# Kernel tuning notes

Hardware: AMD Instinct MI355X
Metric: run time of the kernel (lower is better)

The kernel has to match this reference:

```python
import jax, jax.numpy as jnp
import numpy as np

A, Bc, C, D = 32, 16, 16, 16
K, PAD = 3, 1
KK = K * K
KKA = KK * A            # 288
KKA2 = KKA // 2 + 1     # 145
BSZ, H, W = 4, 14, 14


def unfold(x, k, pad):
    # torch F.unfold ordering: channel-major, kernel-minor -> matches patches
    p = jax.lax.conv_general_dilated_patches(
        x, (k, k), (1, 1), padding=((pad, pad), (pad, pad)),
        dimension_numbers=("NCHW", "OIHW", "NCHW"))
    b, ckk, h, w = p.shape
    return p.reshape(b, ckk, h * w)


def freq_filter(x, cw):
    # x: [bl, kkA, B, D]; shared complex filter over all B splits (Frequency)
    xf = jnp.fft.rfft(x.astype(jnp.float32), axis=1, norm='ortho')  # [bl,kkA2,B,D]
    wc = cw[..., 0] + 1j * cw[..., 1]                               # [kkA2, D]
    y = jnp.fft.irfft(xf * wc[None, :, None, :], n=x.shape[1], axis=1, norm='ortho')
    return y + x


def spatial_gate(logit, gamma, beta, w, bias):
    # logit: [bl, kkA, B]; shared Spatial module applied per B split (vectorized)
    bl, kka, nb = logit.shape
    g = logit.reshape(bl, KK, A, nb)
    mu = g.mean(axis=2, keepdims=True)
    var = g.var(axis=2, keepdims=True)
    g = (g - mu) / jnp.sqrt(var + 1e-5) * gamma[None, None, :, None] + beta[None, None, :, None]
    # conv1d with kernel size 1 == channel mixing over kk
    out = jnp.einsum('oi,biaj->boaj', w, g) + bias[None, :, None, None]
    out = jax.nn.gelu(out, approximate=False)
    return out.reshape(bl, kka, nb) + logit  # residual inside Spatial


def setup_inputs():
    key = jax.random.key(0)
    ks = jax.random.split(key, 8)
    return {
        "a": jax.random.uniform(ks[0], (BSZ, A, H, W), jnp.float32) + 0.1,
        "pose": jax.random.normal(ks[1], (BSZ, A * C, H, W), jnp.float32),
        "mpose_w": jax.random.normal(ks[2], (Bc * D, C), jnp.float32) * 0.05,
        "mpose_b": jnp.zeros((Bc * D,), jnp.float32),
        "cpose2_w": jax.random.normal(ks[3], (Bc, C), jnp.float32) * 0.05,
        "cpose2_b": jnp.zeros((Bc,), jnp.float32),
        "complex_weight": jax.random.normal(ks[4], (KKA2, C, 2), jnp.float32) * 0.02,
        "ln_gamma": jnp.ones((A,), jnp.float32),
        "ln_beta": jnp.zeros((A,), jnp.float32),
        "sp_w": jax.random.normal(ks[5], (KK, KK), jnp.float32) * 0.1,
        "sp_b": jnp.ones((KK,), jnp.float32),
    }


def reference(a, pose, mpose_w, mpose_b, cpose2_w, cpose2_b, complex_weight,
              ln_gamma, ln_beta, sp_w, sp_b):
    b, _, h, w = a.shape
    # ---- unfold pose: [b, A*C*kk, l] -> [b*l, kkA, C]
    pu = unfold(pose, K, PAD)
    l = pu.shape[-1]
    pu = pu.reshape(b, A, C, KK, l).transpose(0, 4, 3, 1, 2).reshape(b * l, KKA, C)
    # ---- pose transform + frequency filter
    p = jax.nn.gelu(pu @ mpose_w.T + mpose_b, approximate=False)
    p = freq_filter(p.reshape(b * l, KKA, Bc, D), complex_weight)
    pose_out = p.reshape(b, l, KKA, Bc, D)
    # ---- routing logits: linear + (spatial gate + residual) added to logit
    logit = pu @ cpose2_w.T + cpose2_b                      # [bl, kkA, B]
    logit = logit + spatial_gate(logit, ln_gamma, ln_beta, sp_w, sp_b)
    r = jax.nn.softmax(logit, axis=2).reshape(b, l, KKA, Bc)
    # ---- unfold activations: [b, l, kkA, 1]
    au = unfold(a, K, PAD).reshape(b, A, KK, l).transpose(0, 3, 2, 1).reshape(b, l, KKA, 1)
    ar = au * r                                             # [b,l,kkA,B]
    ar_sum = ar.sum(axis=2, keepdims=True)                  # [b,l,1,B]
    coeff = (ar / ar_sum)[..., None]                        # [b,l,kkA,B,1]
    a_out = (ar_sum / au.sum(axis=2, keepdims=True)).squeeze(2)  # [b,l,B]
    a_out = a_out.transpose(0, 2, 1).reshape(b, Bc, h, w)
    po = (coeff * pose_out).sum(axis=2).reshape(b, l, Bc * D)
    po = po.transpose(0, 2, 1).reshape(b, Bc * D, h, w)
    return a_out, po
```

## Files before the change

kernel.cpp:

```cpp
#include <hip/hip_runtime.h>
#include <math.h>


typedef __attribute__((ext_vector_type(8))) short bf16x8;
typedef __attribute__((ext_vector_type(4))) float f32x4;

__device__ inline float4 ld4(const float* p) { return *reinterpret_cast<const float4*>(p); }
__device__ inline void st4(float* p, float4 v) { *reinterpret_cast<float4*>(p) = v; }
__device__ inline unsigned short f2bf(float f) {
  union { float f; unsigned int i; } v; v.f = f;
  unsigned int r = v.i + 0x7FFFu + ((v.i >> 16) & 1u);
  return (unsigned short)(r >> 16);
}
__device__ inline float gelu_f(float v) {
  float u = v * 0.70710678118654752f;
  float au = fabsf(u);
  float t = __builtin_amdgcn_rcpf(fmaf(0.3275911f, au, 1.f));
  float poly = t * fmaf(t, fmaf(t, fmaf(t, fmaf(t, 1.061405429f, -1.453152027f),
                                        1.421413741f), -0.284496736f),
                        0.254829592f);
  float e = __expf(-u * u);
  float r = fmaf(-poly, e, 1.f);
  float erfv = copysignf(r, u);
  return 0.5f * v * (1.f + erfv);
}

__global__ __launch_bounds__(256) void k_prep(
    const float* __restrict__ cw, const float* __restrict__ pose,
    const float* __restrict__ a_img, unsigned short* __restrict__ ws_H,
    float* __restrict__ poseT, float* __restrict__ aT) {
  int bid = blockIdx.x, tid = threadIdx.x;
  if (bid < 96) {
    __shared__ float s_h2[576];
    __shared__ float s_cs[288], s_sn[288], s_wr[145], s_wi[145];
    int d = bid / 6, chunk = bid % 6;
    for (int m = tid; m < 288; m += 256) {
      float sn, cs;
      sincosf((float)m * (6.283185307179586f / 288.f), &sn, &cs);
      s_cs[m] = cs; s_sn[m] = sn;
    }
    for (int f = tid; f < 145; f += 256) {
      s_wr[f] = cw[(f * 16 + d) * 2 + 0];
      s_wi[f] = cw[(f * 16 + d) * 2 + 1];
    }
    __syncthreads();
    for (int t = tid; t < 288; t += 256) {
      float acc = s_wr[0] + ((t & 1) ? -s_wr[144] : s_wr[144]);
      for (int f = 1; f < 144; ++f) {
        int m = (f * t) % 288;
        acc = fmaf(2.f * s_wr[f], s_cs[m], acc);
        acc = fmaf(-2.f * s_wi[f], s_sn[m], acc);
      }
      float h = acc * (1.f / 288.f);
      s_h2[t] = h;
      s_h2[t + 288] = h;
    }
    __syncthreads();
    for (int e = tid; e < 13824; e += 256) {
      int j = e & 7, l = (e >> 3) & 63;
      int kk = (e >> 9) % 9, mtl = (e >> 9) / 9;
      int mt = chunk * 3 + mtl;
      int m = l & 15, g = l >> 4;
      int n = kk * 32 + g * 8 + j, t = mt * 16 + m;
      float v = s_h2[n - t + 288] + ((n == t) ? 1.f : 0.f);
      ws_H[d * 82944 + ((mt * 9 + kk) * 64 + l) * 8 + j] = f2bf(v);
    }
  } else {
    __shared__ float s[32 * 201];
    int tb = bid - 96;
    int b = tb / 17, ch = tb % 17;
    const float* src = (ch < 16) ? (pose + (b * 512 + ch * 32) * 196)
                                 : (a_img + b * 32 * 196);
    for (int e = tid; e < 6272; e += 256) {
      int c = e / 196, l = e - c * 196;
      s[c * 201 + l] = src[e];
    }
    __syncthreads();
    if (ch < 16) {
      float* dst = poseT + b * 196 * 512 + ch * 32;
      for (int e = tid; e < 6272; e += 256) {
        int l = e >> 5, c = e & 31;
        dst[l * 512 + c] = s[c * 201 + l];
      }
    } else {
      float* dst = aT + b * 196 * 32;
      for (int e = tid; e < 6272; e += 256) {
        int l = e >> 5, c = e & 31;
        dst[l * 32 + c] = s[c * 201 + l];
      }
    }
  }
}

__global__ __launch_bounds__(256) void k_rowprep(
    const float* __restrict__ poseT, const float* __restrict__ aT,
    const float* __restrict__ cpose2_w, const float* __restrict__ cpose2_b,
    const float* __restrict__ ln_g, const float* __restrict__ ln_b,
    const float* __restrict__ sp_w, const float* __restrict__ sp_b,
    float* __restrict__ out_a, unsigned short* __restrict__ ws_pu,
    unsigned short* __restrict__ ws_cb) {
  __shared__ __align__(16) float s_pu[288 * 20];
#define s_l2 s_pu
  __shared__ __align__(16) float s_lg[288 * 20];
  __shared__ float s_au[288];
  __shared__ float s_mu[144], s_rs[144];
  __shared__ float s_ga[32], s_be[32];
  __shared__ float s_part[256], s_pau[16];
  __shared__ float s_as[16];

  int tid = threadIdx.x;
  int row = blockIdx.x;
  int b = row / 196, loc = row % 196, i0 = loc / 14, j0 = loc % 14;
  int b_ = tid & 15;

  if (tid < 32) { s_ga[tid] = ln_g[tid]; s_be[tid] = ln_b[tid]; }

  float wcol[16];
#pragma unroll
  for (int q = 0; q < 4; ++q) {
    float4 v = ld4(&cpose2_w[b_ * 16 + 4 * q]);
    wcol[4 * q] = v.x; wcol[4 * q + 1] = v.y;
    wcol[4 * q + 2] = v.z; wcol[4 * q + 3] = v.w;
  }
  float cbv = cpose2_b[b_];

  const float* pT = poseT + b * 196 * 512;
  for (int e = tid; e < 1152; e += 256) {
    int q = e & 3, n = e >> 2;
    int kk = n >> 5, a = n & 31;
    int ki = (kk * 11) >> 5, kj = kk - 3 * ki;
    int yy = i0 + ki - 1, xx = j0 + kj - 1;
    float4 v = make_float4(0.f, 0.f, 0.f, 0.f);
    if ((unsigned)yy < 14u && (unsigned)xx < 14u)
      v = ld4(&pT[(yy * 14 + xx) * 512 + a * 16 + q * 4]);
    st4(&s_pu[n * 20 + q * 4], v);
  }
  const float* aTb = aT + b * 196 * 32;
  for (int n = tid; n < 288; n += 256) {
    int kk = n >> 5, a = n & 31;
    int ki = (kk * 11) >> 5, kj = kk - 3 * ki;
    int yy = i0 + ki - 1, xx = j0 + kj - 1;
    float v = 0.f;
    if ((unsigned)yy < 14u && (unsigned)xx < 14u)
      v = aTb[(yy * 14 + xx) * 32 + a];
    s_au[n] = v;
  }
  __syncthreads();

  for (int e = tid; e < 4608; e += 256) {
    int j = e & 7, l2 = (e >> 3) & 31, mt = e >> 8;
    int m = l2 & 15, c = (l2 >> 4) * 8 + j;
    ws_pu[row * 4608 + e] = f2bf(s_pu[(mt * 16 + m) * 20 + c]);
  }

  {
    int n0 = tid >> 4;
#pragma unroll 3
    for (int k = 0; k < 18; ++k) {
      int n = n0 + 16 * k;
      const float* pr = &s_pu[n * 20];
      float acc = cbv;
#pragma unroll
      for (int q = 0; q < 4; ++q) {
        float4 p = ld4(pr + 4 * q);
        acc += p.x * wcol[4 * q] + p.y * wcol[4 * q + 1] +
               p.z * wcol[4 * q + 2] + p.w * wcol[4 * q + 3];
      }
      s_lg[n * 20 + b_] = acc;
    }
  }
  __syncthreads();

  if (tid < 144) {
    int kk = tid >> 4, B = tid & 15;
    float s = 0.f, s2 = 0.f;
    for (int a = 0; a < 32; ++a) {
      float v = s_lg[(kk * 32 + a) * 20 + B];
      s += v; s2 += v * v;
    }
    float mu = s * (1.f / 32.f);
    float var = s2 * (1.f / 32.f) - mu * mu;
    s_mu[tid] = mu;
    s_rs[tid] = rsqrtf(var + 1e-5f);
  } else if (tid < 160) {
    int t2 = tid - 144;
    float p = 0.f;
    for (int i = 0; i < 18; ++i) p += s_au[t2 * 18 + i];
    s_pau[t2] = p;
  }
  __syncthreads();

  {
    float mu9[9], rs9[9];
#pragma unroll
    for (int i2 = 0; i2 < 9; ++i2) {
      mu9[i2] = s_mu[i2 * 16 + b_];
      rs9[i2] = s_rs[i2 * 16 + b_];
    }
#pragma unroll
    for (int half = 0; half < 2; ++half) {
      int a = (tid >> 4) + 16 * half;
      float ga = s_ga[a], be = s_be[a];
      float gn[9], lg9[9];
#pragma unroll
      for (int i2 = 0; i2 < 9; ++i2) {
        float v = s_lg[(i2 * 32 + a) * 20 + b_];
        lg9[i2] = v;
        gn[i2] = (v - mu9[i2]) * rs9[i2] * ga + be;
      }
#pragma unroll
      for (int o = 0; o < 9; ++o) {
        float acc = sp_b[o];
#pragma unroll
        for (int i2 = 0; i2 < 9; ++i2) acc += sp_w[o * 9 + i2] * gn[i2];
        s_l2[(o * 32 + a) * 20 + b_] = 2.f * lg9[o] + gelu_f(acc);
      }
    }
  }
  __syncthreads();

  for (int n = tid; n < 288; n += 256) {
    float v[16];
#pragma unroll
    for (int q = 0; q < 4; ++q) {
      float4 t = ld4(&s_l2[n * 20 + 4 * q]);
      v[4 * q] = t.x; v[4 * q + 1] = t.y; v[4 * q + 2] = t.z; v[4 * q + 3] = t.w;
    }
    float m = v[0];
#pragma unroll
    for (int e = 1; e < 16; ++e) m = fmaxf(m, v[e]);
    float s = 0.f;
#pragma unroll
    for (int e = 0; e < 16; ++e) { v[e] = __expf(v[e] - m); s += v[e]; }
    float inv = 1.f / s;
#pragma unroll
    for (int q = 0; q < 4; ++q)
      st4(&s_l2[n * 20 + 4 * q],
          make_float4(v[4 * q] * inv, v[4 * q + 1] * inv, v[4 * q + 2] * inv,
                      v[4 * q + 3] * inv));
  }
  __syncthreads();

  {
    int sl = tid >> 4;
    float part = 0.f;
#pragma unroll 3
    for (int i = 0; i < 18; ++i) {
      int n = sl * 18 + i;
      part += s_au[n] * s_l2[n * 20 + b_];
    }
    s_part[tid] = part;
  }
  __syncthreads();

  if (tid < 16) {
    float s = 0.f;
#pragma unroll
    for (int q = 0; q < 16; ++q) s += s_part[tid + 16 * q];
    s_as[tid] = s;
    float aus = 0.f;
#pragma unroll
    for (int q = 0; q < 16; ++q) aus += s_pau[q];
    out_a[(b * 16 + tid) * 196 + loc] = s / aus;
  }
  __syncthreads();

  {
    float inv_as = 1.f / s_as[(tid >> 3) & 15];
    for (int e = tid; e < 4608; e += 256) {
      int j = e & 7, B = (e >> 3) & 15, g2 = (e >> 7) & 3, kk = e >> 9;
      int n = kk * 32 + g2 * 8 + j;
      float v = s_au[n] * s_l2[n * 20 + B] * inv_as;
      ws_cb[row * 4608 + e] = f2bf(v);
    }
  }
#undef s_l2
}

__global__ __launch_bounds__(256, 3) void k_gterm(
    const unsigned short* __restrict__ ws_H,
    const unsigned short* __restrict__ ws_pu,
    const unsigned short* __restrict__ ws_cb,
    const float* __restrict__ mpose_w, const float* __restrict__ mpose_b,
    float* __restrict__ out_po) {
  int bid = blockIdx.x;
  int xcd = bid & 7, q = bid >> 3;
  int k13 = q % 13, d = q / 13;
  int ro = xcd + 8 * k13;
  if (ro >= 98) return;

  int tid = threadIdx.x;
  int w = tid >> 6, l = tid & 63;
  int row0 = ro * 8 + w * 2, row1 = row0 + 1;
  int b_ = l & 15, g = l >> 4;

  const bf16x8 z8 = {0, 0, 0, 0, 0, 0, 0, 0};
  const f32x4 zf = {0.f, 0.f, 0.f, 0.f};

  bf16x8 bmw = z8;
  if (g < 2) {
    const float* mp = mpose_w + (b_ * 16 + d) * 16 + g * 8;
#pragma unroll
    for (int j = 0; j < 8; ++j) bmw[j] = (short)f2bf(mp[j]);
  }
  float mb = mpose_b[b_ * 16 + d];

  union CU { uint4 u; bf16x8 v; };
  CU c0[9], c1[9];
  {
    const uint4* gC0 = (const uint4*)ws_cb + row0 * 576;
    const uint4* gC1 = (const uint4*)ws_cb + row1 * 576;
#pragma unroll
    for (int kk = 0; kk < 9; ++kk) {
      c0[kk].u = gC0[kk * 64 + l];
      c1[kk].u = gC1[kk * 64 + l];
    }
#pragma unroll
    for (int kk = 0; kk < 9; ++kk) {
      asm volatile("" : "+v"(c0[kk].u.x), "+v"(c0[kk].u.y),
                        "+v"(c0[kk].u.z), "+v"(c0[kk].u.w));
      asm volatile("" : "+v"(c1[kk].u.x), "+v"(c1[kk].u.y),
                        "+v"(c1[kk].u.z), "+v"(c1[kk].u.w));
    }
  }
  const bf16x8* aP0 = (const bf16x8*)ws_pu + row0 * 576;
  const bf16x8* aP1 = (const bf16x8*)ws_pu + row1 * 576;
  const bf16x8* aH = (const bf16x8*)ws_H + d * 10368;

  bf16x8 an0 = z8, an1 = z8;
  if (g < 2) { an0 = aP0[l]; an1 = aP1[l]; }

  float po0 = 0.f, po1 = 0.f;
  for (int mt = 0; mt < 18; ++mt) {
    bf16x8 h[9];
#pragma unroll
    for (int kk = 0; kk < 9; ++kk) h[kk] = aH[(mt * 9 + kk) * 64 + l];
    bf16x8 a0 = an0, a1 = an1;
    if (mt < 17 && g < 2) {
      an0 = aP0[(mt + 1) * 32 + l];
      an1 = aP1[(mt + 1) * 32 + l];
    }
    __builtin_amdgcn_s_setprio(1);
    f32x4 xp0 = __builtin_amdgcn_mfma_f32_16x16x32_bf16(a0, bmw, zf, 0, 0, 0);
    f32x4 xp1 = __builtin_amdgcn_mfma_f32_16x16x32_bf16(a1, bmw, zf, 0, 0, 0);
    f32x4 g0a = zf, g0b = zf, g1a = zf, g1b = zf;
#pragma unroll
    for (int kp = 0; kp < 4; ++kp) {
      g0a = __builtin_amdgcn_mfma_f32_16x16x32_bf16(h[2 * kp], c0[2 * kp].v, g0a, 0, 0, 0);
      g1a = __builtin_amdgcn_mfma_f32_16x16x32_bf16(h[2 * kp], c1[2 * kp].v, g1a, 0, 0, 0);
      g0b = __builtin_amdgcn_mfma_f32_16x16x32_bf16(h[2 * kp + 1], c0[2 * kp + 1].v, g0b, 0, 0, 0);
      g1b = __builtin_amdgcn_mfma_f32_16x16x32_bf16(h[2 * kp + 1], c1[2 * kp + 1].v, g1b, 0, 0, 0);
    }
    g0a = __builtin_amdgcn_mfma_f32_16x16x32_bf16(h[8], c0[8].v, g0a, 0, 0, 0);
    g1a = __builtin_amdgcn_mfma_f32_16x16x32_bf16(h[8], c1[8].v, g1a, 0, 0, 0);
    __builtin_amdgcn_s_setprio(0);
#pragma unroll
    for (int r = 0; r < 4; ++r) {
      float s0 = xp0[r] + mb, s1 = xp1[r] + mb;
      float x0 = gelu_f(s0), x1 = gelu_f(s1);
      po0 = fmaf(g0a[r], x0, po0);
      po0 = fmaf(g0b[r], x0, po0);
      po1 = fmaf(g1a[r], x1, po1);
      po1 = fmaf(g1b[r], x1, po1);
    }
  }

  po0 += __shfl_xor(po0, 16);
  po0 += __shfl_xor(po0, 32);
  po1 += __shfl_xor(po1, 16);
  po1 += __shfl_xor(po1, 32);
  if (l < 16) {
    int bb = row0 / 196, lc0 = row0 % 196, lc1 = row1 % 196;
    out_po[((bb * 256) + l * 16 + d) * 196 + lc0] = po0;
    out_po[((bb * 256) + l * 16 + d) * 196 + lc1] = po1;
  }
}

extern "C" void kernel_launch(void* const* d_in, const int* in_sizes, int n_in,
                              void* d_out, int out_size, void* d_ws, size_t ws_size,
                              hipStream_t stream) {
  const float* a_img    = (const float*)d_in[0];
  const float* pose     = (const float*)d_in[1];
  const float* mpose_w  = (const float*)d_in[2];
  const float* mpose_b  = (const float*)d_in[3];
  const float* cpose2_w = (const float*)d_in[4];
  const float* cpose2_b = (const float*)d_in[5];
  const float* cw       = (const float*)d_in[6];
  const float* ln_g     = (const float*)d_in[7];
  const float* ln_b     = (const float*)d_in[8];
  const float* sp_w     = (const float*)d_in[9];
  const float* sp_b     = (const float*)d_in[10];

  float* out = (float*)d_out;
  float* poseT  = (float*)d_ws;
  float* aT     = poseT + 4 * 196 * 512;
  unsigned short* ws_H  = (unsigned short*)(aT + 4 * 196 * 32);
  unsigned short* ws_pu = ws_H + 16 * 82944;
  unsigned short* ws_cb = ws_pu + 784 * 4608;

  hipLaunchKernelGGL(k_prep, dim3(164), dim3(256), 0, stream,
                     cw, pose, a_img, ws_H, poseT, aT);
  hipLaunchKernelGGL(k_rowprep, dim3(784), dim3(256), 0, stream,
                     poseT, aT, cpose2_w, cpose2_b, ln_g, ln_b, sp_w, sp_b,
                     out, ws_pu, ws_cb);
  hipLaunchKernelGGL(k_gterm, dim3(1664), dim3(256), 0, stream,
                     ws_H, ws_pu, ws_cb, mpose_w, mpose_b, out + 12544);
}
```

Measured before the change: 117.8 us.

## Remap rowprep rows to match gterm XCD layout and simplify MFMA chains

k_rowprep now uses the same XCD-aware block-to-row mapping as k_gterm, so each row's ws_pu/ws_cb data is written on the XCD whose L2 will later read it. Its grid grows to 832 blocks, with the excess blocks exiting early. In k_gterm the bias is folded into the MFMA accumulator input. The two interleaved accumulator chains are merged into one serial chain of 9 MFMAs per row, and setprio is removed. The single chain lengthens MFMA dependency latency while cutting register use and a few adds.

```diff
diff --git a/kernel.cpp b/kernel.cpp
--- a/kernel.cpp
+++ b/kernel.cpp
@@ -108,8 +108,13 @@
   __shared__ float s_part[256], s_pau[16];
   __shared__ float s_as[16];
 
+  int bid = blockIdx.x;
+  int x = bid & 7, j = bid >> 3;
+  int o = x + 8 * (j % 13);
+  if (o >= 98) return;
+  int row = o * 8 + (j / 13);
+
   int tid = threadIdx.x;
-  int row = blockIdx.x;
   int b = row / 196, loc = row % 196, i0 = loc / 14, j0 = loc % 14;
   int b_ = tid & 15;
 
@@ -148,8 +153,8 @@
   __syncthreads();
 
   for (int e = tid; e < 4608; e += 256) {
-    int j = e & 7, l2 = (e >> 3) & 31, mt = e >> 8;
-    int m = l2 & 15, c = (l2 >> 4) * 8 + j;
+    int jj = e & 7, l2 = (e >> 3) & 31, mt = e >> 8;
+    int m = l2 & 15, c = (l2 >> 4) * 8 + jj;
     ws_pu[row * 4608 + e] = f2bf(s_pu[(mt * 16 + m) * 20 + c]);
   }
 
@@ -209,11 +214,11 @@
         gn[i2] = (v - mu9[i2]) * rs9[i2] * ga + be;
       }
 #pragma unroll
-      for (int o = 0; o < 9; ++o) {
-        float acc = sp_b[o];
-#pragma unroll
-        for (int i2 = 0; i2 < 9; ++i2) acc += sp_w[o * 9 + i2] * gn[i2];
-        s_l2[(o * 32 + a) * 20 + b_] = 2.f * lg9[o] + gelu_f(acc);
+      for (int oo = 0; oo < 9; ++oo) {
+        float acc = sp_b[oo];
+#pragma unroll
+        for (int i2 = 0; i2 < 9; ++i2) acc += sp_w[oo * 9 + i2] * gn[i2];
+        s_l2[(oo * 32 + a) * 20 + b_] = 2.f * lg9[oo] + gelu_f(acc);
       }
     }
   }
@@ -268,8 +273,8 @@
   {
     float inv_as = 1.f / s_as[(tid >> 3) & 15];
     for (int e = tid; e < 4608; e += 256) {
-      int j = e & 7, B = (e >> 3) & 15, g2 = (e >> 7) & 3, kk = e >> 9;
-      int n = kk * 32 + g2 * 8 + j;
+      int jj = e & 7, B = (e >> 3) & 15, g2 = (e >> 7) & 3, kk = e >> 9;
+      int n = kk * 32 + g2 * 8 + jj;
       float v = s_au[n] * s_l2[n * 20 + B] * inv_as;
       ws_cb[row * 4608 + e] = f2bf(v);
     }
@@ -301,9 +306,10 @@
   if (g < 2) {
     const float* mp = mpose_w + (b_ * 16 + d) * 16 + g * 8;
 #pragma unroll
-    for (int j = 0; j < 8; ++j) bmw[j] = (short)f2bf(mp[j]);
+    for (int jj = 0; jj < 8; ++jj) bmw[jj] = (short)f2bf(mp[jj]);
   }
   float mb = mpose_b[b_ * 16 + d];
+  f32x4 mbv = {mb, mb, mb, mb};
 
   union CU { uint4 u; bf16x8 v; };
   CU c0[9], c1[9];
@@ -340,28 +346,18 @@
       an0 = aP0[(mt + 1) * 32 + l];
       an1 = aP1[(mt + 1) * 32 + l];
     }
-    __builtin_amdgcn_s_setprio(1);
-    f32x4 xp0 = __builtin_amdgcn_mfma_f32_16x16x32_bf16(a0, bmw, zf, 0, 0, 0);
-    f32x4 xp1 = __builtin_amdgcn_mfma_f32_16x16x32_bf16(a1, bmw, zf, 0, 0, 0);
-    f32x4 g0a = zf, g0b = zf, g1a = zf, g1b = zf;
-#pragma unroll
-    for (int kp = 0; kp < 4; ++kp) {
-      g0a = __builtin_amdgcn_mfma_f32_16x16x32_bf16(h[2 * kp], c0[2 * kp].v, g0a, 0, 0, 0);
-      g1a = __builtin_amdgcn_mfma_f32_16x16x32_bf16(h[2 * kp], c1[2 * kp].v, g1a, 0, 0, 0);
-      g0b = __builtin_amdgcn_mfma_f32_16x16x32_bf16(h[2 * kp + 1], c0[2 * kp + 1].v, g0b, 0, 0, 0);
-      g1b = __builtin_amdgcn_mfma_f32_16x16x32_bf16(h[2 * kp + 1], c1[2 * kp + 1].v, g1b, 0, 0, 0);
-    }
-    g0a = __builtin_amdgcn_mfma_f32_16x16x32_bf16(h[8], c0[8].v, g0a, 0, 0, 0);
-    g1a = __builtin_amdgcn_mfma_f32_16x16x32_bf16(h[8], c1[8].v, g1a, 0, 0, 0);
-    __builtin_amdgcn_s_setprio(0);
+    f32x4 xp0 = __builtin_amdgcn_mfma_f32_16x16x32_bf16(a0, bmw, mbv, 0, 0, 0);
+    f32x4 xp1 = __builtin_amdgcn_mfma_f32_16x16x32_bf16(a1, bmw, mbv, 0, 0, 0);
+    f32x4 g0 = zf, g1 = zf;
+#pragma unroll
+    for (int kk = 0; kk < 9; ++kk) {
+      g0 = __builtin_amdgcn_mfma_f32_16x16x32_bf16(h[kk], c0[kk].v, g0, 0, 0, 0);
+      g1 = __builtin_amdgcn_mfma_f32_16x16x32_bf16(h[kk], c1[kk].v, g1, 0, 0, 0);
+    }
 #pragma unroll
     for (int r = 0; r < 4; ++r) {
-      float s0 = xp0[r] + mb, s1 = xp1[r] + mb;
-      float x0 = gelu_f(s0), x1 = gelu_f(s1);
-      po0 = fmaf(g0a[r], x0, po0);
-      po0 = fmaf(g0b[r], x0, po0);
-      po1 = fmaf(g1a[r], x1, po1);
-      po1 = fmaf(g1b[r], x1, po1);
+      po0 += g0[r] * gelu_f(xp0[r]);
+      po1 += g1[r] * gelu_f(xp1[r]);
     }
   }
 
@@ -400,7 +396,7 @@
 
   hipLaunchKernelGGL(k_prep, dim3(164), dim3(256), 0, stream,
                      cw, pose, a_img, ws_H, poseT, aT);
-  hipLaunchKernelGGL(k_rowprep, dim3(784), dim3(256), 0, stream,
+  hipLaunchKernelGGL(k_rowprep, dim3(832), dim3(256), 0, stream,
                      poseT, aT, cpose2_w, cpose2_b, ln_g, ln_b, sp_w, sp_b,
                      out, ws_pu, ws_cb);
   hipLaunchKernelGGL(k_gterm, dim3(1664), dim3(256), 0, stream,
```

Result: faster. 109.5 us (-7.0%).
